# Performance work log

Measured on AMD Instinct MI355X. Metric: run time of the kernel, lower is better.

## Reference

```python
import jax, jax.numpy as jnp
import numpy as np

EPS = 1e-06


def setup_inputs() -> dict:
    key = jax.random.key(0)
    ks = jax.random.split(key, 6)
    B, L, N = 64, 4096, 128
    F = L // 2 + 1  # 2049 rfft bins
    E = 8
    x = jax.random.normal(ks[0], (B, L, N), dtype=jnp.float32)
    band_boundaries = jax.random.normal(ks[1], (E - 1,), dtype=jnp.float32)
    # gate: Linear(F,F) -> ReLU -> Linear(F,E); stored as [in,out] matrices
    gate_w1 = jax.random.normal(ks[2], (F, F), dtype=jnp.float32) * (1.0 / np.sqrt(F))
    gate_b1 = jnp.zeros((F,), dtype=jnp.float32)
    gate_w2 = jax.random.normal(ks[3], (F, E), dtype=jnp.float32) * (1.0 / np.sqrt(F))
    gate_b2 = jnp.zeros((E,), dtype=jnp.float32)
    return {"x": x, "band_boundaries": band_boundaries,
            "gate_w1": gate_w1, "gate_b1": gate_b1,
            "gate_w2": gate_w2, "gate_b2": gate_b2}


def reference(x, band_boundaries, gate_w1, gate_b1, gate_w2, gate_b2):
    # FrequencyMoE forward (residual_add=True). x: [B, L, N]
    B, L, N = x.shape
    F = L // 2 + 1
    xN = jnp.transpose(x, (0, 2, 1))  # [B, N, L]
    mean = jnp.mean(xN, axis=-1, keepdims=True)
    var = jnp.var(xN, axis=-1, keepdims=True) + EPS
    # NOTE: original code computes x_norm then overwrites with xN (normalization skipped),
    # but still rescales the reconstruction by sqrt(var) and adds mean back. Faithful copy.
    freq = jnp.fft.rfft(xN, n=L, axis=-1)  # [B, N, F] complex64

    # learnable band boundaries -> integer bin indices (non-differentiable, as in torch .long())
    bb = jnp.sort(jax.nn.sigmoid(band_boundaries))
    b01 = jnp.concatenate([jnp.zeros((1,), bb.dtype), bb, jnp.ones((1,), bb.dtype)])
    idx = jnp.clip((b01 * F).astype(jnp.int32), 0, F)
    idx = idx.at[-1].set(F)  # [E+1]

    bins = jnp.arange(F)
    # per-expert frequency masks [E, F]: bin in [idx[e], idx[e+1])
    masks = ((bins[None, :] >= idx[:-1, None]) & (bins[None, :] < idx[1:, None])).astype(xN.dtype)

    # gating on mean magnitude spectrum over variables
    mag = jnp.mean(jnp.abs(freq), axis=1)  # [B, F]
    h = jax.nn.relu(mag @ gate_w1 + gate_b1)
    weights = jax.nn.softmax(h @ gate_w2 + gate_b2, axis=-1)  # [B, E]

    # fused weighted-mask combination: sum_e w[b,e]*mask[e,f] applied to spectrum
    wmask = weights @ masks  # [B, F]
    freq_out = freq * wmask[:, None, :]
    x_rec = jnp.fft.irfft(freq_out, n=L, axis=-1)  # [B, N, L]
    x_rec = x_rec * jnp.sqrt(var) + mean
    outN = xN + x_rec  # residual_add=True
    return jnp.transpose(outN, (0, 2, 1))  # [B, L, N]
```

## Files before the change

### kernel.cpp

```cpp
#include <hip/hip_runtime.h>

#define B_ 64
#define L_ 4096
#define N_ 128
#define F_ 2049
#define M_ 2048

__device__ __forceinline__ int pidx(int a) { return a + (a >> 3); }

__device__ __forceinline__ float2 cadd(float2 a, float2 b) { return make_float2(a.x + b.x, a.y + b.y); }
__device__ __forceinline__ float2 csub(float2 a, float2 b) { return make_float2(a.x - b.x, a.y - b.y); }
__device__ __forceinline__ float2 cmul(float2 a, float2 b) {
  return make_float2(a.x * b.x - a.y * b.y, a.x * b.y + a.y * b.x);
}
template <int SGN>
__device__ __forceinline__ float2 mulsi(float2 a) {
  return (SGN > 0) ? make_float2(-a.y, a.x) : make_float2(a.y, -a.x);
}

template <int SGN>
__device__ __forceinline__ void dft8(float2* v) {
  const float C = 0.70710678118654752f;
  float2 t0 = cadd(v[0], v[4]), t1 = csub(v[0], v[4]);
  float2 t2 = cadd(v[2], v[6]), t3 = mulsi<SGN>(csub(v[2], v[6]));
  float2 t4 = cadd(v[1], v[5]), t5 = csub(v[1], v[5]);
  float2 t6 = cadd(v[3], v[7]), t7 = mulsi<SGN>(csub(v[3], v[7]));
  float2 u0 = cadd(t0, t2), u1 = csub(t0, t2);
  float2 u2 = cadd(t1, t3), u3 = csub(t1, t3);
  float2 u4 = cadd(t4, t6), u5 = csub(t4, t6);
  float2 u6 = cadd(t5, t7), u7 = csub(t5, t7);
  float2 w1 = make_float2(C, (SGN > 0) ? C : -C);
  float2 w3 = make_float2(-C, (SGN > 0) ? C : -C);
  float2 a5 = mulsi<SGN>(u5);
  float2 b6 = cmul(u6, w1);
  float2 b7 = cmul(u7, w3);
  v[0] = cadd(u0, u4); v[4] = csub(u0, u4);
  v[2] = cadd(u1, a5); v[6] = csub(u1, a5);
  v[1] = cadd(u2, b6); v[5] = csub(u2, b6);
  v[3] = cadd(u3, b7); v[7] = csub(u3, b7);
}

template <int SGN>
__device__ __forceinline__ void dft4(float2* v) {
  float2 e0 = cadd(v[0], v[2]), e1 = csub(v[0], v[2]);
  float2 o0 = cadd(v[1], v[3]), o1 = mulsi<SGN>(csub(v[1], v[3]));
  v[0] = cadd(e0, o0); v[2] = csub(e0, o0);
  v[1] = cadd(e1, o1); v[3] = csub(e1, o1);
}

template <int SGN>
__device__ __forceinline__ void tw8(float2* v, int pm) {
  float ang = (float)pm * 0.00306796157577128245f;
  float sv, cv;
  __sincosf(ang, &sv, &cv);
  float2 w = make_float2(cv, (SGN > 0) ? sv : -sv);
  float2 wk = w;
  v[1] = cmul(v[1], wk);
#pragma unroll
  for (int k = 2; k < 8; ++k) { wk = cmul(wk, w); v[k] = cmul(v[k], wk); }
}

template <int SGN>
__device__ __forceinline__ void fft2048(float2* __restrict__ buf, float2* v, int t) {
  dft8<SGN>(v);
  tw8<SGN>(v, t);
  __syncthreads();
#pragma unroll
  for (int k = 0; k < 8; ++k) buf[pidx(8 * t + k)] = v[k];
  __syncthreads();
#pragma unroll
  for (int r = 0; r < 8; ++r) v[r] = buf[pidx(t + 256 * r)];
  dft8<SGN>(v);
  tw8<SGN>(v, t & ~7);
  __syncthreads();
  {
    int q = t & 7, p = t >> 3;
#pragma unroll
    for (int k = 0; k < 8; ++k) buf[pidx(q + 8 * (8 * p + k))] = v[k];
  }
  __syncthreads();
#pragma unroll
  for (int r = 0; r < 8; ++r) v[r] = buf[pidx(t + 256 * r)];
  dft8<SGN>(v);
  tw8<SGN>(v, t & ~63);
  __syncthreads();
  {
    int q = t & 63, p = t >> 6;
#pragma unroll
    for (int k = 0; k < 8; ++k) buf[pidx(q + 64 * (8 * p + k))] = v[k];
  }
  __syncthreads();
  float2 w0[4], w1s[4];
#pragma unroll
  for (int r = 0; r < 4; ++r) {
    w0[r] = buf[pidx(t + 512 * r)];
    w1s[r] = buf[pidx(t + 256 + 512 * r)];
  }
  dft4<SGN>(w0);
  dft4<SGN>(w1s);
  __syncthreads();
#pragma unroll
  for (int k = 0; k < 4; ++k) {
    buf[pidx(t + 512 * k)] = w0[k];
    buf[pidx(t + 256 + 512 * k)] = w1s[k];
  }
  __syncthreads();
}

__global__ __launch_bounds__(256) void transpose4_k(const float* __restrict__ in,
                                                    float* __restrict__ out,
                                                    int R, int C) {
  __shared__ float tile[64][65];
  const float* ip = in + (size_t)blockIdx.z * R * C;
  float* op = out + (size_t)blockIdx.z * R * C;
  int c0 = blockIdx.x * 64;
  int r0 = blockIdx.y * 64;
  int t = threadIdx.x;
  {
    int fx = t & 15;
    int rq = t >> 4;
#pragma unroll
    for (int i = 0; i < 4; ++i) {
      int r = rq + 16 * i;
      float4 v = *(const float4*)&ip[(size_t)(r0 + r) * C + (c0 + 4 * fx)];
      tile[r][4 * fx + 0] = v.x;
      tile[r][4 * fx + 1] = v.y;
      tile[r][4 * fx + 2] = v.z;
      tile[r][4 * fx + 3] = v.w;
    }
  }
  __syncthreads();
  {
    int gm = t & 15;
    int cq = t >> 4;
#pragma unroll
    for (int i = 0; i < 4; ++i) {
      int c = cq + 16 * i;
      float4 v;
      v.x = tile[4 * gm + 0][c];
      v.y = tile[4 * gm + 1][c];
      v.z = tile[4 * gm + 2][c];
      v.w = tile[4 * gm + 3][c];
      *(float4*)&op[(size_t)(c0 + c) * R + (r0 + 4 * gm)] = v;
    }
  }
}

template <int S>
__global__ __launch_bounds__(256) void p1_fft_mag(const float* __restrict__ src,
                                                  float* __restrict__ magsum) {
  __shared__ float2 buf[2304];
  int t = threadIdx.x;
  int blk = blockIdx.x;
  int b = blk >> 7;
  int n = blk & 127;
  const float* base = (S == 1) ? (src + (size_t)blk * L_)
                               : (src + (size_t)b * L_ * N_ + n);
  float2 v[8];
  if (S == 1) {
    const float2* r2 = (const float2*)base;
#pragma unroll
    for (int r = 0; r < 8; ++r) v[r] = r2[t + 256 * r];
  } else {
#pragma unroll
    for (int r = 0; r < 8; ++r) {
      int k = t + 256 * r;
      v[r] = make_float2(base[(size_t)(2 * k) * S], base[(size_t)(2 * k + 1) * S]);
    }
  }
  fft2048<-1>(buf, v, t);

  float* msum = magsum + (size_t)b * F_;
#pragma unroll
  for (int i = 0; i < 8; ++i) {
    int f = t + 256 * i;
    float mg;
    if (f == 0) {
      float2 z = buf[pidx(0)];
      mg = fabsf(z.x + z.y);
      atomicAdd(&msum[2048], fabsf(z.x - z.y));
    } else {
      float2 zf = buf[pidx(f)], zm = buf[pidx(2048 - f)];
      float Are = 0.5f * (zf.x + zm.x), Aim = 0.5f * (zf.y - zm.y);
      float Bre = 0.5f * (zf.y + zm.y), Bim = -0.5f * (zf.x - zm.x);
      float ang = (float)f * 0.00153398078788564117f;
      float sv, cv;
      __sincosf(ang, &sv, &cv);
      float Xre = Are + cv * Bre + sv * Bim;
      float Xim = Aim + cv * Bim - sv * Bre;
      mg = sqrtf(Xre * Xre + Xim * Xim);
    }
    atomicAdd(&msum[f], mg);
  }
}

__global__ __launch_bounds__(256) void p1_fft_mag_z(const float* __restrict__ src,
                                                    float2* __restrict__ zout,
                                                    float* __restrict__ magsum) {
  __shared__ float2 buf[2304];
  int t = threadIdx.x;
  int blk = blockIdx.x;
  int b = blk >> 7;
  const float2* r2 = (const float2*)(src + (size_t)blk * L_);
  float2 v[8];
#pragma unroll
  for (int r = 0; r < 8; ++r) v[r] = r2[t + 256 * r];
  fft2048<-1>(buf, v, t);

  float* msum = magsum + (size_t)b * F_;
  float2* zrow = zout + (size_t)blk * (size_t)M_;
#pragma unroll
  for (int i = 0; i < 4; ++i) {
    int f = t + 256 * i;
    if (f == 0) {
      float2 z = buf[pidx(0)];
      float2 zc = buf[pidx(1024)];
      zrow[0] = z;
      zrow[1024] = zc;
      atomicAdd(&msum[0], fabsf(z.x + z.y));
      atomicAdd(&msum[2048], fabsf(z.x - z.y));
      atomicAdd(&msum[1024], sqrtf(zc.x * zc.x + zc.y * zc.y));
    } else {
      float2 zf = buf[pidx(f)], zm = buf[pidx(2048 - f)];
      zrow[f] = zf;
      zrow[2048 - f] = zm;
      float Are = 0.5f * (zf.x + zm.x), Aim = 0.5f * (zf.y - zm.y);
      float Bre = 0.5f * (zf.y + zm.y), Bim = -0.5f * (zf.x - zm.x);
      float ang = (float)f * 0.00153398078788564117f;
      float sv, cv;
      __sincosf(ang, &sv, &cv);
      float WBre = cv * Bre + sv * Bim;
      float WBim = cv * Bim - sv * Bre;
      float Xre = Are + WBre, Xim = Aim + WBim;
      float Xmre = Are - WBre, Xmim = Aim - WBim;
      atomicAdd(&msum[f], sqrtf(Xre * Xre + Xim * Xim));
      atomicAdd(&msum[2048 - f], sqrtf(Xmre * Xmre + Xmim * Xmim));
    }
  }
}

__global__ __launch_bounds__(256) void magt_k(const float* __restrict__ mag,
                                              float* __restrict__ magT) {
  int idx = blockIdx.x * 256 + threadIdx.x;
  if (idx >= 64 * F_) return;
  int f = idx >> 6, b = idx & 63;
  magT[idx] = mag[(size_t)b * F_ + f] * (1.0f / 128.0f);
}

#define G1K 33
__global__ __launch_bounds__(256) void g1_gemm(const float* __restrict__ magT,
                                               const float* __restrict__ W1,
                                               float* __restrict__ hsum) {
  int o = blockIdx.x * 256 + threadIdx.x;
  if (o >= F_) return;
  int i0 = blockIdx.y * G1K;
  int i1 = min(F_, i0 + G1K);
  float acc[64];
#pragma unroll
  for (int b = 0; b < 64; ++b) acc[b] = 0.f;
  for (int i = i0; i < i1; ++i) {
    float w = W1[(size_t)i * F_ + o];
    const float* mrow = magT + (size_t)i * 64;
#pragma unroll
    for (int b = 0; b < 64; ++b) acc[b] = fmaf(mrow[b], w, acc[b]);
  }
#pragma unroll
  for (int b = 0; b < 64; ++b) atomicAdd(&hsum[(size_t)b * F_ + o], acc[b]);
}

__global__ __launch_bounds__(256) void g2_gate(const float* __restrict__ hsum,
                                               const float* __restrict__ gb1,
                                               const float* __restrict__ W2,
                                               const float* __restrict__ gb2,
                                               const float* __restrict__ bbs,
                                               float* __restrict__ wmask) {
  __shared__ float red[256 * 8];
  __shared__ float wsm[8];
  __shared__ int idxs[9];
  int b = blockIdx.x;
  int t = threadIdx.x;
  float p[8];
#pragma unroll
  for (int e = 0; e < 8; ++e) p[e] = 0.f;
  for (int o = t; o < F_; o += 256) {
    float hv = hsum[(size_t)b * F_ + o] + gb1[o];
    hv = fmaxf(hv, 0.f);
    const float4* w2p = (const float4*)(W2 + (size_t)o * 8);
    float4 wa = w2p[0], wb = w2p[1];
    p[0] += hv * wa.x; p[1] += hv * wa.y; p[2] += hv * wa.z; p[3] += hv * wa.w;
    p[4] += hv * wb.x; p[5] += hv * wb.y; p[6] += hv * wb.z; p[7] += hv * wb.w;
  }
#pragma unroll
  for (int e = 0; e < 8; ++e) red[t * 8 + e] = p[e];
  __syncthreads();
  for (int s = 128; s >= 1; s >>= 1) {
    if (t < s) {
#pragma unroll
      for (int e = 0; e < 8; ++e) red[t * 8 + e] += red[(t + s) * 8 + e];
    }
    __syncthreads();
  }
  if (t == 0) {
    float lg[8];
    float mx = -1e30f;
#pragma unroll
    for (int e = 0; e < 8; ++e) { lg[e] = red[e] + gb2[e]; mx = fmaxf(mx, lg[e]); }
    float sm = 0.f;
#pragma unroll
    for (int e = 0; e < 8; ++e) { lg[e] = expf(lg[e] - mx); sm += lg[e]; }
    float inv = 1.f / sm;
#pragma unroll
    for (int e = 0; e < 8; ++e) wsm[e] = lg[e] * inv;
    float bv[7];
#pragma unroll
    for (int k = 0; k < 7; ++k) bv[k] = 1.f / (1.f + expf(-bbs[k]));
    for (int a = 1; a < 7; ++a) {
      float v = bv[a];
      int j = a - 1;
      while (j >= 0 && bv[j] > v) { bv[j + 1] = bv[j]; --j; }
      bv[j + 1] = v;
    }
    idxs[0] = 0;
    idxs[8] = F_;
    for (int k = 0; k < 7; ++k) {
      int v = (int)(bv[k] * (float)F_);
      v = min(max(v, 0), F_);
      idxs[k + 1] = v;
    }
  }
  __syncthreads();
  for (int f = t; f < F_; f += 256) {
    float wv = 0.f;
#pragma unroll
    for (int e = 0; e < 8; ++e)
      if (f >= idxs[e] && f < idxs[e + 1]) wv = wsm[e];
    wmask[(size_t)b * F_ + f] = wv;
  }
}

__global__ __launch_bounds__(256) void p3_filter_z(float2* __restrict__ zbuf,
                                                   const float* __restrict__ wmask) {
  __shared__ float2 buf[2304];
  __shared__ float rb[8];
  __shared__ float sstat[2];
  int t = threadIdx.x;
  int blk = blockIdx.x;
  int b = blk >> 7;
  float2* zrow = zbuf + (size_t)blk * (size_t)M_;
  float2 v[8];
  float lsq = 0.f;
#pragma unroll
  for (int r = 0; r < 8; ++r) {
    float2 z = zrow[t + 256 * r];
    v[r] = z;
    lsq += z.x * z.x + z.y * z.y;
  }
#pragma unroll
  for (int r = 0; r < 8; ++r) buf[pidx(t + 256 * r)] = v[r];
  for (int off = 32; off > 0; off >>= 1) lsq += __shfl_down(lsq, off);
  {
    int lane = t & 63, wid = t >> 6;
    if (lane == 0) rb[wid] = lsq;
  }
  __syncthreads();
  if (t == 0) {
    float s2 = rb[0] + rb[1] + rb[2] + rb[3];
    float2 z0 = buf[pidx(0)];
    float mean = (z0.x + z0.y) * (1.0f / 4096.0f);
    float sumsq = s2 * (1.0f / 2048.0f);
    float var = sumsq * (1.0f / 4096.0f) - mean * mean + 1e-6f;
    sstat[0] = mean;
    sstat[1] = sqrtf(var);
  }
  __syncthreads();

  float mean = sstat[0], sdv = sstat[1];
  const float* wm = wmask + (size_t)b * F_;

  float2 zf_[4], zm_[4];
#pragma unroll
  for (int i = 0; i < 4; ++i) {
    int f = t + 256 * i;
    int fm = (f == 0) ? 1024 : (2048 - f);
    zf_[i] = buf[pidx(f)];
    zm_[i] = buf[pidx(fm)];
  }
  __syncthreads();
#pragma unroll
  for (int i = 0; i < 4; ++i) {
    int f = t + 256 * i;
    if (f == 0) {
      float2 z0 = zf_[0];
      float2 zc = zm_[0];
      float X0 = (z0.x + z0.y) * (1.f + sdv * wm[0]);
      float XM = (z0.x - z0.y) * (1.f + sdv * wm[2048]);
      buf[pidx(0)] = make_float2(0.5f * (X0 + XM), 0.5f * (X0 - XM));
      float mc = 1.f + sdv * wm[1024];
      buf[pidx(1024)] = make_float2(zc.x * mc, zc.y * mc);
    } else {
      float2 zf = zf_[i], zm = zm_[i];
      float Are = 0.5f * (zf.x + zm.x), Aim = 0.5f * (zf.y - zm.y);
      float Bre = 0.5f * (zf.y + zm.y), Bim = -0.5f * (zf.x - zm.x);
      float ang = (float)f * 0.00153398078788564117f;
      float sv, cv;
      __sincosf(ang, &sv, &cv);
      float WBre = cv * Bre + sv * Bim;
      float WBim = cv * Bim - sv * Bre;
      float Xre = Are + WBre, Xim = Aim + WBim;
      float Xmre = Are - WBre, Xmim = -(Aim - WBim);
      float mf = 1.f + sdv * wm[f];
      float mg = 1.f + sdv * wm[2048 - f];
      Xre *= mf; Xim *= mf;
      Xmre *= mg; Xmim *= mg;
      float Apre = 0.5f * (Xre + Xmre), Apim = 0.5f * (Xim - Xmim);
      float Tre = 0.5f * (Xre - Xmre), Tim = 0.5f * (Xim + Xmim);
      float Bpre = cv * Tre - sv * Tim;
      float Bpim = cv * Tim + sv * Tre;
      buf[pidx(f)] = make_float2(Apre - Bpim, Apim + Bpre);
      float Agre = 0.5f * (Xmre + Xre), Agim = 0.5f * (Xmim - Xim);
      float Tgre = 0.5f * (Xmre - Xre), Tgim = 0.5f * (Xmim + Xim);
      float Bgre = -(cv * Tgre + sv * Tgim);
      float Bgim = -(cv * Tgim - sv * Tgre);
      buf[pidx(2048 - f)] = make_float2(Agre - Bgim, Agim + Bgre);
    }
  }
  __syncthreads();
#pragma unroll
  for (int r = 0; r < 8; ++r) v[r] = buf[pidx(t + 256 * r)];
  fft2048<1>(buf, v, t);

  const float inv = 1.0f / 2048.0f;
#pragma unroll
  for (int r = 0; r < 8; ++r) {
    int k = t + 256 * r;
    float2 z = buf[pidx(k)];
    zrow[k] = make_float2(z.x * inv + mean, z.y * inv + mean);
  }
}

template <int S>
__global__ __launch_bounds__(256) void p3_filter(const float* __restrict__ src,
                                                 const float* __restrict__ wmask,
                                                 float* __restrict__ dstp) {
  __shared__ float2 buf[2304];
  __shared__ float sstat[2];
  int t = threadIdx.x;
  int blk = blockIdx.x;
  int b = blk >> 7;
  int n = blk & 127;
  const float* base = (S == 1) ? (src + (size_t)blk * L_)
                               : (src + (size_t)b * L_ * N_ + n);
  float* obase = (S == 1) ? (dstp + (size_t)blk * L_)
                          : (dstp + (size_t)b * L_ * N_ + n);
  float2 v[8];
  float lsum = 0.f, lsq = 0.f;
  if (S == 1) {
    const float2* r2 = (const float2*)base;
#pragma unroll
    for (int r = 0; r < 8; ++r) {
      float2 z = r2[t + 256 * r];
      v[r] = z;
      lsum += z.x + z.y;
      lsq += z.x * z.x + z.y * z.y;
    }
  } else {
#pragma unroll
    for (int r = 0; r < 8; ++r) {
      int k = t + 256 * r;
      float2 z = make_float2(base[(size_t)(2 * k) * S], base[(size_t)(2 * k + 1) * S]);
      v[r] = z;
      lsum += z.x + z.y;
      lsq += z.x * z.x + z.y * z.y;
    }
  }
  for (int off = 32; off > 0; off >>= 1) {
    lsum += __shfl_down(lsum, off);
    lsq += __shfl_down(lsq, off);
  }
  {
    float* rb = (float*)buf;
    int lane = t & 63, wid = t >> 6;
    if (lane == 0) { rb[wid] = lsum; rb[8 + wid] = lsq; }
    __syncthreads();
    if (t == 0) {
      float s1 = rb[0] + rb[1] + rb[2] + rb[3];
      float s2 = rb[8] + rb[9] + rb[10] + rb[11];
      float mean = s1 * (1.0f / 4096.0f);
      float var = s2 * (1.0f / 4096.0f) - mean * mean + 1e-6f;
      sstat[0] = mean;
      sstat[1] = sqrtf(var);
    }
  }
  fft2048<-1>(buf, v, t);

  float mean = sstat[0], sdv = sstat[1];
  const float* wm = wmask + (size_t)b * F_;

  float2 zf_[4], zm_[4];
#pragma unroll
  for (int i = 0; i < 4; ++i) {
    int f = t + 256 * i;
    int fm = (f == 0) ? 1024 : (2048 - f);
    zf_[i] = buf[pidx(f)];
    zm_[i] = buf[pidx(fm)];
  }
  __syncthreads();
#pragma unroll
  for (int i = 0; i < 4; ++i) {
    int f = t + 256 * i;
    if (f == 0) {
      float2 z0 = zf_[0];
      float2 zc = zm_[0];
      float X0 = (z0.x + z0.y) * (1.f + sdv * wm[0]);
      float XM = (z0.x - z0.y) * (1.f + sdv * wm[2048]);
      buf[pidx(0)] = make_float2(0.5f * (X0 + XM), 0.5f * (X0 - XM));
      float mc = 1.f + sdv * wm[1024];
      buf[pidx(1024)] = make_float2(zc.x * mc, zc.y * mc);
    } else {
      float2 zf = zf_[i], zm = zm_[i];
      float Are = 0.5f * (zf.x + zm.x), Aim = 0.5f * (zf.y - zm.y);
      float Bre = 0.5f * (zf.y + zm.y), Bim = -0.5f * (zf.x - zm.x);
      float ang = (float)f * 0.00153398078788564117f;
      float sv, cv;
      __sincosf(ang, &sv, &cv);
      float WBre = cv * Bre + sv * Bim;
      float WBim = cv * Bim - sv * Bre;
      float Xre = Are + WBre, Xim = Aim + WBim;
      float Xmre = Are - WBre, Xmim = -(Aim - WBim);
      float mf = 1.f + sdv * wm[f];
      float mg = 1.f + sdv * wm[2048 - f];
      Xre *= mf; Xim *= mf;
      Xmre *= mg; Xmim *= mg;
      float Apre = 0.5f * (Xre + Xmre), Apim = 0.5f * (Xim - Xmim);
      float Tre = 0.5f * (Xre - Xmre), Tim = 0.5f * (Xim + Xmim);
      float Bpre = cv * Tre - sv * Tim;
      float Bpim = cv * Tim + sv * Tre;
      buf[pidx(f)] = make_float2(Apre - Bpim, Apim + Bpre);
      float Agre = 0.5f * (Xmre + Xre), Agim = 0.5f * (Xmim - Xim);
      float Tgre = 0.5f * (Xmre - Xre), Tgim = 0.5f * (Xmim + Xim);
      float Bgre = -(cv * Tgre + sv * Tgim);
      float Bgim = -(cv * Tgim - sv * Tgre);
      buf[pidx(2048 - f)] = make_float2(Agre - Bgim, Agim + Bgre);
    }
  }
  __syncthreads();
#pragma unroll
  for (int r = 0; r < 8; ++r) v[r] = buf[pidx(t + 256 * r)];
  fft2048<1>(buf, v, t);

  const float inv = 1.0f / 2048.0f;
  if (S == 1) {
    float2* o2 = (float2*)obase;
#pragma unroll
    for (int r = 0; r < 8; ++r) {
      int k = t + 256 * r;
      float2 z = buf[pidx(k)];
      o2[k] = make_float2(z.x * inv + mean, z.y * inv + mean);
    }
  } else {
#pragma unroll
    for (int r = 0; r < 8; ++r) {
      int k = t + 256 * r;
      float2 z = buf[pidx(k)];
      obase[(size_t)(2 * k) * S] = z.x * inv + mean;
      obase[(size_t)(2 * k + 1) * S] = z.y * inv + mean;
    }
  }
}

extern "C" void kernel_launch(void* const* d_in, const int* in_sizes, int n_in,
                              void* d_out, int out_size, void* d_ws,
                              size_t ws_size, hipStream_t stream) {
  const float* x = (const float*)d_in[0];
  const float* bbs = (const float*)d_in[1];
  const float* W1 = (const float*)d_in[2];
  const float* gb1 = (const float*)d_in[3];
  const float* W2 = (const float*)d_in[4];
  const float* gb2 = (const float*)d_in[5];
  float* out = (float*)d_out;

  const size_t bigElems = (size_t)B_ * N_ * L_;
  const size_t smallBytes = (size_t)3 * B_ * F_ * sizeof(float);
  const bool fast = ws_size >= bigElems * sizeof(float) + smallBytes;

  char* smallBase = (char*)d_ws + (fast ? bigElems * sizeof(float) : 0);
  float* magsum = (float*)smallBase;
  float* hsum = magsum + (size_t)B_ * F_;
  float* wmaskp = hsum + (size_t)B_ * F_;

  hipMemsetAsync(magsum, 0, (size_t)2 * B_ * F_ * sizeof(float), stream);

  const int g1x = (F_ + 255) / 256;
  const int g1y = (F_ + G1K - 1) / G1K;
  const int mtb = (64 * F_ + 255) / 256;
  if (fast) {
    float2* Z = (float2*)d_ws;
    transpose4_k<<<dim3(N_ / 64, L_ / 64, B_), 256, 0, stream>>>(x, out, L_, N_);
    p1_fft_mag_z<<<dim3(B_ * N_), 256, 0, stream>>>(out, Z, magsum);
    magt_k<<<dim3(mtb), 256, 0, stream>>>(magsum, wmaskp);
    g1_gemm<<<dim3(g1x, g1y), 256, 0, stream>>>(wmaskp, W1, hsum);
    g2_gate<<<dim3(B_), 256, 0, stream>>>(hsum, gb1, W2, gb2, bbs, wmaskp);
    p3_filter_z<<<dim3(B_ * N_), 256, 0, stream>>>(Z, wmaskp);
    transpose4_k<<<dim3(L_ / 64, N_ / 64, B_), 256, 0, stream>>>((float*)d_ws, out, N_, L_);
  } else {
    p1_fft_mag<N_><<<dim3(B_ * N_), 256, 0, stream>>>(x, magsum);
    magt_k<<<dim3(mtb), 256, 0, stream>>>(magsum, wmaskp);
    g1_gemm<<<dim3(g1x, g1y), 256, 0, stream>>>(wmaskp, W1, hsum);
    g2_gate<<<dim3(B_), 256, 0, stream>>>(hsum, gb1, W2, gb2, bbs, wmaskp);
    p3_filter<N_><<<dim3(B_ * N_), 256, 0, stream>>>(x, wmaskp, out);
  }
}
```

Measured before the change: 497.7 us.

## Process two FFT rows per block to share twiddles, syncs, and atomics

The forward and inverse FFT kernels now handle two rows per 256-thread block, interleaving two independent FFTs with shared twiddle computation and shared barriers. The magnitude atomics are combined across both rows, halving the atomic count, and the filter's separate register staging pass with its extra barrier is removed by operating in place on shared memory. This roughly doubles register and shared-memory use per block (launch bounds now request 4 blocks per CU) in exchange for more instruction-level parallelism and fewer barriers per row.

```diff
diff --git a/kernel.cpp b/kernel.cpp
--- a/kernel.cpp
+++ b/kernel.cpp
@@ -49,16 +49,20 @@
 }
 
 template <int SGN>
-__device__ __forceinline__ void tw8(float2* v, int pm) {
+__device__ __forceinline__ float2 twroot(int pm) {
   float ang = (float)pm * 0.00306796157577128245f;
   float sv, cv;
   __sincosf(ang, &sv, &cv);
-  float2 w = make_float2(cv, (SGN > 0) ? sv : -sv);
+  return make_float2(cv, (SGN > 0) ? sv : -sv);
+}
+__device__ __forceinline__ void tw8w(float2* v, float2 w) {
   float2 wk = w;
   v[1] = cmul(v[1], wk);
 #pragma unroll
   for (int k = 2; k < 8; ++k) { wk = cmul(wk, w); v[k] = cmul(v[k], wk); }
 }
+template <int SGN>
+__device__ __forceinline__ void tw8(float2* v, int pm) { tw8w(v, twroot<SGN>(pm)); }
 
 template <int SGN>
 __device__ __forceinline__ void fft2048(float2* __restrict__ buf, float2* v, int t) {
@@ -103,6 +107,63 @@
   for (int k = 0; k < 4; ++k) {
     buf[pidx(t + 512 * k)] = w0[k];
     buf[pidx(t + 256 + 512 * k)] = w1s[k];
+  }
+  __syncthreads();
+}
+
+template <int SGN>
+__device__ __forceinline__ void fft2048x2(float2* __restrict__ bufA, float2* __restrict__ bufB,
+                                          float2* va, float2* vb, int t) {
+  dft8<SGN>(va); dft8<SGN>(vb);
+  { float2 w = twroot<SGN>(t); tw8w(va, w); tw8w(vb, w); }
+  __syncthreads();
+#pragma unroll
+  for (int k = 0; k < 8; ++k) { bufA[pidx(8 * t + k)] = va[k]; bufB[pidx(8 * t + k)] = vb[k]; }
+  __syncthreads();
+#pragma unroll
+  for (int r = 0; r < 8; ++r) { va[r] = bufA[pidx(t + 256 * r)]; vb[r] = bufB[pidx(t + 256 * r)]; }
+  dft8<SGN>(va); dft8<SGN>(vb);
+  { float2 w = twroot<SGN>(t & ~7); tw8w(va, w); tw8w(vb, w); }
+  __syncthreads();
+  {
+    int q = t & 7, p = t >> 3;
+#pragma unroll
+    for (int k = 0; k < 8; ++k) {
+      int a = pidx(q + 8 * (8 * p + k));
+      bufA[a] = va[k]; bufB[a] = vb[k];
+    }
+  }
+  __syncthreads();
+#pragma unroll
+  for (int r = 0; r < 8; ++r) { va[r] = bufA[pidx(t + 256 * r)]; vb[r] = bufB[pidx(t + 256 * r)]; }
+  dft8<SGN>(va); dft8<SGN>(vb);
+  { float2 w = twroot<SGN>(t & ~63); tw8w(va, w); tw8w(vb, w); }
+  __syncthreads();
+  {
+    int q = t & 63, p = t >> 6;
+#pragma unroll
+    for (int k = 0; k < 8; ++k) {
+      int a = pidx(q + 64 * (8 * p + k));
+      bufA[a] = va[k]; bufB[a] = vb[k];
+    }
+  }
+  __syncthreads();
+  float2 wA0[4], wA1[4], wB0[4], wB1[4];
+#pragma unroll
+  for (int r = 0; r < 4; ++r) {
+    wA0[r] = bufA[pidx(t + 512 * r)];
+    wA1[r] = bufA[pidx(t + 256 + 512 * r)];
+    wB0[r] = bufB[pidx(t + 512 * r)];
+    wB1[r] = bufB[pidx(t + 256 + 512 * r)];
+  }
+  dft4<SGN>(wA0); dft4<SGN>(wA1); dft4<SGN>(wB0); dft4<SGN>(wB1);
+  __syncthreads();
+#pragma unroll
+  for (int k = 0; k < 4; ++k) {
+    bufA[pidx(t + 512 * k)] = wA0[k];
+    bufA[pidx(t + 256 + 512 * k)] = wA1[k];
+    bufB[pidx(t + 512 * k)] = wB0[k];
+    bufB[pidx(t + 256 + 512 * k)] = wB1[k];
   }
   __syncthreads();
 }
@@ -194,47 +255,60 @@
   }
 }
 
-__global__ __launch_bounds__(256) void p1_fft_mag_z(const float* __restrict__ src,
-                                                    float2* __restrict__ zout,
-                                                    float* __restrict__ magsum) {
-  __shared__ float2 buf[2304];
+__global__ __launch_bounds__(256, 4) void p1_fft_mag_z2(const float* __restrict__ src,
+                                                        float2* __restrict__ zout,
+                                                        float* __restrict__ magsum) {
+  __shared__ float2 bufA[2304];
+  __shared__ float2 bufB[2304];
   int t = threadIdx.x;
   int blk = blockIdx.x;
-  int b = blk >> 7;
-  const float2* r2 = (const float2*)(src + (size_t)blk * L_);
-  float2 v[8];
-#pragma unroll
-  for (int r = 0; r < 8; ++r) v[r] = r2[t + 256 * r];
-  fft2048<-1>(buf, v, t);
+  int b = blk >> 6;
+  const float2* rA = (const float2*)(src + (size_t)(2 * blk) * L_);
+  const float2* rB = rA + M_;
+  float2 va[8], vb[8];
+#pragma unroll
+  for (int r = 0; r < 8; ++r) { va[r] = rA[t + 256 * r]; vb[r] = rB[t + 256 * r]; }
+  fft2048x2<-1>(bufA, bufB, va, vb, t);
 
   float* msum = magsum + (size_t)b * F_;
-  float2* zrow = zout + (size_t)blk * (size_t)M_;
+  float2* zrA = zout + (size_t)(2 * blk) * (size_t)M_;
+  float2* zrB = zrA + M_;
 #pragma unroll
   for (int i = 0; i < 4; ++i) {
     int f = t + 256 * i;
     if (f == 0) {
-      float2 z = buf[pidx(0)];
-      float2 zc = buf[pidx(1024)];
-      zrow[0] = z;
-      zrow[1024] = zc;
-      atomicAdd(&msum[0], fabsf(z.x + z.y));
-      atomicAdd(&msum[2048], fabsf(z.x - z.y));
-      atomicAdd(&msum[1024], sqrtf(zc.x * zc.x + zc.y * zc.y));
+      float2 zA = bufA[pidx(0)], zcA = bufA[pidx(1024)];
+      float2 zB = bufB[pidx(0)], zcB = bufB[pidx(1024)];
+      zrA[0] = zA; zrA[1024] = zcA;
+      zrB[0] = zB; zrB[1024] = zcB;
+      atomicAdd(&msum[0], fabsf(zA.x + zA.y) + fabsf(zB.x + zB.y));
+      atomicAdd(&msum[2048], fabsf(zA.x - zA.y) + fabsf(zB.x - zB.y));
+      atomicAdd(&msum[1024], sqrtf(zcA.x * zcA.x + zcA.y * zcA.y) +
+                             sqrtf(zcB.x * zcB.x + zcB.y * zcB.y));
     } else {
-      float2 zf = buf[pidx(f)], zm = buf[pidx(2048 - f)];
-      zrow[f] = zf;
-      zrow[2048 - f] = zm;
-      float Are = 0.5f * (zf.x + zm.x), Aim = 0.5f * (zf.y - zm.y);
-      float Bre = 0.5f * (zf.y + zm.y), Bim = -0.5f * (zf.x - zm.x);
+      float2 zfA = bufA[pidx(f)], zmA = bufA[pidx(2048 - f)];
+      float2 zfB = bufB[pidx(f)], zmB = bufB[pidx(2048 - f)];
+      zrA[f] = zfA; zrA[2048 - f] = zmA;
+      zrB[f] = zfB; zrB[2048 - f] = zmB;
       float ang = (float)f * 0.00153398078788564117f;
       float sv, cv;
       __sincosf(ang, &sv, &cv);
+      float Are = 0.5f * (zfA.x + zmA.x), Aim = 0.5f * (zfA.y - zmA.y);
+      float Bre = 0.5f * (zfA.y + zmA.y), Bim = -0.5f * (zfA.x - zmA.x);
       float WBre = cv * Bre + sv * Bim;
       float WBim = cv * Bim - sv * Bre;
-      float Xre = Are + WBre, Xim = Aim + WBim;
-      float Xmre = Are - WBre, Xmim = Aim - WBim;
-      atomicAdd(&msum[f], sqrtf(Xre * Xre + Xim * Xim));
-      atomicAdd(&msum[2048 - f], sqrtf(Xmre * Xmre + Xmim * Xmim));
+      float XreA = Are + WBre, XimA = Aim + WBim;
+      float XmreA = Are - WBre, XmimA = Aim - WBim;
+      float Cre = 0.5f * (zfB.x + zmB.x), Cim = 0.5f * (zfB.y - zmB.y);
+      float Dre = 0.5f * (zfB.y + zmB.y), Dim = -0.5f * (zfB.x - zmB.x);
+      float WDre = cv * Dre + sv * Dim;
+      float WDim = cv * Dim - sv * Dre;
+      float XreB = Cre + WDre, XimB = Cim + WDim;
+      float XmreB = Cre - WDre, XmimB = Cim - WDim;
+      atomicAdd(&msum[f], sqrtf(XreA * XreA + XimA * XimA) +
+                          sqrtf(XreB * XreB + XimB * XimB));
+      atomicAdd(&msum[2048 - f], sqrtf(XmreA * XmreA + XmimA * XmimA) +
+                                 sqrtf(XmreB * XmreB + XmimB * XmimB));
     }
   }
 }
@@ -338,103 +412,134 @@
   }
 }
 
-__global__ __launch_bounds__(256) void p3_filter_z(float2* __restrict__ zbuf,
-                                                   const float* __restrict__ wmask) {
-  __shared__ float2 buf[2304];
-  __shared__ float rb[8];
-  __shared__ float sstat[2];
+__device__ __forceinline__ void filter_pair(float2& zf, float2& zm, int f,
+                                            float cv, float sv,
+                                            float mf, float mg) {
+  float Are = 0.5f * (zf.x + zm.x), Aim = 0.5f * (zf.y - zm.y);
+  float Bre = 0.5f * (zf.y + zm.y), Bim = -0.5f * (zf.x - zm.x);
+  float WBre = cv * Bre + sv * Bim;
+  float WBim = cv * Bim - sv * Bre;
+  float Xre = Are + WBre, Xim = Aim + WBim;
+  float Xmre = Are - WBre, Xmim = -(Aim - WBim);
+  Xre *= mf; Xim *= mf;
+  Xmre *= mg; Xmim *= mg;
+  float Apre = 0.5f * (Xre + Xmre), Apim = 0.5f * (Xim - Xmim);
+  float Tre = 0.5f * (Xre - Xmre), Tim = 0.5f * (Xim + Xmim);
+  float Bpre = cv * Tre - sv * Tim;
+  float Bpim = cv * Tim + sv * Tre;
+  zf = make_float2(Apre - Bpim, Apim + Bpre);
+  float Agre = 0.5f * (Xmre + Xre), Agim = 0.5f * (Xmim - Xim);
+  float Tgre = 0.5f * (Xmre - Xre), Tgim = 0.5f * (Xmim + Xim);
+  float Bgre = -(cv * Tgre + sv * Tgim);
+  float Bgim = -(cv * Tgim - sv * Tgre);
+  zm = make_float2(Agre - Bgim, Agim + Bgre);
+}
+
+__global__ __launch_bounds__(256, 4) void p3_filter_z2(float2* __restrict__ zbuf,
+                                                       const float* __restrict__ wmask) {
+  __shared__ float2 bufA[2304];
+  __shared__ float2 bufB[2304];
+  __shared__ float rb[16];
+  __shared__ float sstat[4];
   int t = threadIdx.x;
   int blk = blockIdx.x;
-  int b = blk >> 7;
-  float2* zrow = zbuf + (size_t)blk * (size_t)M_;
-  float2 v[8];
-  float lsq = 0.f;
+  int b = blk >> 6;
+  float2* zrA = zbuf + (size_t)(2 * blk) * (size_t)M_;
+  float2* zrB = zrA + M_;
+  float2 va[8], vb[8];
+  float lsqA = 0.f, lsqB = 0.f;
 #pragma unroll
   for (int r = 0; r < 8; ++r) {
-    float2 z = zrow[t + 256 * r];
-    v[r] = z;
-    lsq += z.x * z.x + z.y * z.y;
-  }
-#pragma unroll
-  for (int r = 0; r < 8; ++r) buf[pidx(t + 256 * r)] = v[r];
-  for (int off = 32; off > 0; off >>= 1) lsq += __shfl_down(lsq, off);
+    float2 zA = zrA[t + 256 * r];
+    float2 zB = zrB[t + 256 * r];
+    va[r] = zA; vb[r] = zB;
+    lsqA += zA.x * zA.x + zA.y * zA.y;
+    lsqB += zB.x * zB.x + zB.y * zB.y;
+  }
+#pragma unroll
+  for (int r = 0; r < 8; ++r) {
+    bufA[pidx(t + 256 * r)] = va[r];
+    bufB[pidx(t + 256 * r)] = vb[r];
+  }
+  for (int off = 32; off > 0; off >>= 1) {
+    lsqA += __shfl_down(lsqA, off);
+    lsqB += __shfl_down(lsqB, off);
+  }
   {
     int lane = t & 63, wid = t >> 6;
-    if (lane == 0) rb[wid] = lsq;
-  }
-  __syncthreads();
-  if (t == 0) {
-    float s2 = rb[0] + rb[1] + rb[2] + rb[3];
-    float2 z0 = buf[pidx(0)];
+    if (lane == 0) { rb[wid] = lsqA; rb[8 + wid] = lsqB; }
+  }
+  __syncthreads();
+  if (t < 2) {
+    const float* rr = rb + 8 * t;
+    float s2 = rr[0] + rr[1] + rr[2] + rr[3];
+    float2 z0 = (t == 0) ? bufA[pidx(0)] : bufB[pidx(0)];
     float mean = (z0.x + z0.y) * (1.0f / 4096.0f);
     float sumsq = s2 * (1.0f / 2048.0f);
     float var = sumsq * (1.0f / 4096.0f) - mean * mean + 1e-6f;
-    sstat[0] = mean;
-    sstat[1] = sqrtf(var);
-  }
-  __syncthreads();
-
-  float mean = sstat[0], sdv = sstat[1];
+    sstat[2 * t] = mean;
+    sstat[2 * t + 1] = sqrtf(var);
+  }
+  __syncthreads();
+
+  float meanA = sstat[0], sdvA = sstat[1];
+  float meanB = sstat[2], sdvB = sstat[3];
   const float* wm = wmask + (size_t)b * F_;
 
-  float2 zf_[4], zm_[4];
-#pragma unroll
-  for (int i = 0; i < 4; ++i) {
-    int f = t + 256 * i;
-    int fm = (f == 0) ? 1024 : (2048 - f);
-    zf_[i] = buf[pidx(f)];
-    zm_[i] = buf[pidx(fm)];
-  }
-  __syncthreads();
 #pragma unroll
   for (int i = 0; i < 4; ++i) {
     int f = t + 256 * i;
     if (f == 0) {
-      float2 z0 = zf_[0];
-      float2 zc = zm_[0];
-      float X0 = (z0.x + z0.y) * (1.f + sdv * wm[0]);
-      float XM = (z0.x - z0.y) * (1.f + sdv * wm[2048]);
-      buf[pidx(0)] = make_float2(0.5f * (X0 + XM), 0.5f * (X0 - XM));
-      float mc = 1.f + sdv * wm[1024];
-      buf[pidx(1024)] = make_float2(zc.x * mc, zc.y * mc);
+      float w0 = wm[0], wN = wm[2048], wC = wm[1024];
+      {
+        float2 z0 = bufA[pidx(0)], zc = bufA[pidx(1024)];
+        float X0 = (z0.x + z0.y) * (1.f + sdvA * w0);
+        float XM = (z0.x - z0.y) * (1.f + sdvA * wN);
+        bufA[pidx(0)] = make_float2(0.5f * (X0 + XM), 0.5f * (X0 - XM));
+        float mc = 1.f + sdvA * wC;
+        bufA[pidx(1024)] = make_float2(zc.x * mc, zc.y * mc);
+      }
+      {
+        float2 z0 = bufB[pidx(0)], zc = bufB[pidx(1024)];
+        float X0 = (z0.x + z0.y) * (1.f + sdvB * w0);
+        float XM = (z0.x - z0.y) * (1.f + sdvB * wN);
+        bufB[pidx(0)] = make_float2(0.5f * (X0 + XM), 0.5f * (X0 - XM));
+        float mc = 1.f + sdvB * wC;
+        bufB[pidx(1024)] = make_float2(zc.x * mc, zc.y * mc);
+      }
     } else {
-      float2 zf = zf_[i], zm = zm_[i];
-      float Are = 0.5f * (zf.x + zm.x), Aim = 0.5f * (zf.y - zm.y);
-      float Bre = 0.5f * (zf.y + zm.y), Bim = -0.5f * (zf.x - zm.x);
       float ang = (float)f * 0.00153398078788564117f;
       float sv, cv;
       __sincosf(ang, &sv, &cv);
-      float WBre = cv * Bre + sv * Bim;
-      float WBim = cv * Bim - sv * Bre;
-      float Xre = Are + WBre, Xim = Aim + WBim;
-      float Xmre = Are - WBre, Xmim = -(Aim - WBim);
-      float mf = 1.f + sdv * wm[f];
-      float mg = 1.f + sdv * wm[2048 - f];
-      Xre *= mf; Xim *= mf;
-      Xmre *= mg; Xmim *= mg;
-      float Apre = 0.5f * (Xre + Xmre), Apim = 0.5f * (Xim - Xmim);
-      float Tre = 0.5f * (Xre - Xmre), Tim = 0.5f * (Xim + Xmim);
-      float Bpre = cv * Tre - sv * Tim;
-      float Bpim = cv * Tim + sv * Tre;
-      buf[pidx(f)] = make_float2(Apre - Bpim, Apim + Bpre);
-      float Agre = 0.5f * (Xmre + Xre), Agim = 0.5f * (Xmim - Xim);
-      float Tgre = 0.5f * (Xmre - Xre), Tgim = 0.5f * (Xmim + Xim);
-      float Bgre = -(cv * Tgre + sv * Tgim);
-      float Bgim = -(cv * Tgim - sv * Tgre);
-      buf[pidx(2048 - f)] = make_float2(Agre - Bgim, Agim + Bgre);
-    }
-  }
-  __syncthreads();
-#pragma unroll
-  for (int r = 0; r < 8; ++r) v[r] = buf[pidx(t + 256 * r)];
-  fft2048<1>(buf, v, t);
+      float wf = wm[f], wg = wm[2048 - f];
+      {
+        float2 zf = bufA[pidx(f)], zm = bufA[pidx(2048 - f)];
+        filter_pair(zf, zm, f, cv, sv, 1.f + sdvA * wf, 1.f + sdvA * wg);
+        bufA[pidx(f)] = zf; bufA[pidx(2048 - f)] = zm;
+      }
+      {
+        float2 zf = bufB[pidx(f)], zm = bufB[pidx(2048 - f)];
+        filter_pair(zf, zm, f, cv, sv, 1.f + sdvB * wf, 1.f + sdvB * wg);
+        bufB[pidx(f)] = zf; bufB[pidx(2048 - f)] = zm;
+      }
+    }
+  }
+  __syncthreads();
+#pragma unroll
+  for (int r = 0; r < 8; ++r) {
+    va[r] = bufA[pidx(t + 256 * r)];
+    vb[r] = bufB[pidx(t + 256 * r)];
+  }
+  fft2048x2<1>(bufA, bufB, va, vb, t);
 
   const float inv = 1.0f / 2048.0f;
 #pragma unroll
   for (int r = 0; r < 8; ++r) {
     int k = t + 256 * r;
-    float2 z = buf[pidx(k)];
-    zrow[k] = make_float2(z.x * inv + mean, z.y * inv + mean);
+    float2 zA = bufA[pidx(k)];
+    float2 zB = bufB[pidx(k)];
+    zrA[k] = make_float2(zA.x * inv + meanA, zA.y * inv + meanA);
+    zrB[k] = make_float2(zB.x * inv + meanB, zB.y * inv + meanB);
   }
 }
 
@@ -496,51 +601,24 @@
   float mean = sstat[0], sdv = sstat[1];
   const float* wm = wmask + (size_t)b * F_;
 
-  float2 zf_[4], zm_[4];
-#pragma unroll
-  for (int i = 0; i < 4; ++i) {
-    int f = t + 256 * i;
-    int fm = (f == 0) ? 1024 : (2048 - f);
-    zf_[i] = buf[pidx(f)];
-    zm_[i] = buf[pidx(fm)];
-  }
-  __syncthreads();
 #pragma unroll
   for (int i = 0; i < 4; ++i) {
     int f = t + 256 * i;
     if (f == 0) {
-      float2 z0 = zf_[0];
-      float2 zc = zm_[0];
+      float2 z0 = buf[pidx(0)];
+      float2 zc = buf[pidx(1024)];
       float X0 = (z0.x + z0.y) * (1.f + sdv * wm[0]);
       float XM = (z0.x - z0.y) * (1.f + sdv * wm[2048]);
       buf[pidx(0)] = make_float2(0.5f * (X0 + XM), 0.5f * (X0 - XM));
       float mc = 1.f + sdv * wm[1024];
       buf[pidx(1024)] = make_float2(zc.x * mc, zc.y * mc);
     } else {
-      float2 zf = zf_[i], zm = zm_[i];
-      float Are = 0.5f * (zf.x + zm.x), Aim = 0.5f * (zf.y - zm.y);
-      float Bre = 0.5f * (zf.y + zm.y), Bim = -0.5f * (zf.x - zm.x);
       float ang = (float)f * 0.00153398078788564117f;
       float sv, cv;
       __sincosf(ang, &sv, &cv);
-      float WBre = cv * Bre + sv * Bim;
-      float WBim = cv * Bim - sv * Bre;
-      float Xre = Are + WBre, Xim = Aim + WBim;
-      float Xmre = Are - WBre, Xmim = -(Aim - WBim);
-      float mf = 1.f + sdv * wm[f];
-      float mg = 1.f + sdv * wm[2048 - f];
-      Xre *= mf; Xim *= mf;
-      Xmre *= mg; Xmim *= mg;
-      float Apre = 0.5f * (Xre + Xmre), Apim = 0.5f * (Xim - Xmim);
-      float Tre = 0.5f * (Xre - Xmre), Tim = 0.5f * (Xim + Xmim);
-      float Bpre = cv * Tre - sv * Tim;
-      float Bpim = cv * Tim + sv * Tre;
-      buf[pidx(f)] = make_float2(Apre - Bpim, Apim + Bpre);
-      float Agre = 0.5f * (Xmre + Xre), Agim = 0.5f * (Xmim - Xim);
-      float Tgre = 0.5f * (Xmre - Xre), Tgim = 0.5f * (Xmim + Xim);
-      float Bgre = -(cv * Tgre + sv * Tgim);
-      float Bgim = -(cv * Tgim - sv * Tgre);
-      buf[pidx(2048 - f)] = make_float2(Agre - Bgim, Agim + Bgre);
+      float2 zf = buf[pidx(f)], zm = buf[pidx(2048 - f)];
+      filter_pair(zf, zm, f, cv, sv, 1.f + sdv * wm[f], 1.f + sdv * wm[2048 - f]);
+      buf[pidx(f)] = zf; buf[pidx(2048 - f)] = zm;
     }
   }
   __syncthreads();
@@ -596,11 +674,11 @@
   if (fast) {
     float2* Z = (float2*)d_ws;
     transpose4_k<<<dim3(N_ / 64, L_ / 64, B_), 256, 0, stream>>>(x, out, L_, N_);
-    p1_fft_mag_z<<<dim3(B_ * N_), 256, 0, stream>>>(out, Z, magsum);
+    p1_fft_mag_z2<<<dim3(B_ * N_ / 2), 256, 0, stream>>>(out, Z, magsum);
     magt_k<<<dim3(mtb), 256, 0, stream>>>(magsum, wmaskp);
     g1_gemm<<<dim3(g1x, g1y), 256, 0, stream>>>(wmaskp, W1, hsum);
     g2_gate<<<dim3(B_), 256, 0, stream>>>(hsum, gb1, W2, gb2, bbs, wmaskp);
-    p3_filter_z<<<dim3(B_ * N_), 256, 0, stream>>>(Z, wmaskp);
+    p3_filter_z2<<<dim3(B_ * N_ / 2), 256, 0, stream>>>(Z, wmaskp);
     transpose4_k<<<dim3(L_ / 64, N_ / 64, B_), 256, 0, stream>>>((float*)d_ws, out, N_, L_);
   } else {
     p1_fft_mag<N_><<<dim3(B_ * N_), 256, 0, stream>>>(x, magsum);
```

Result: faster. 473.8 us (-4.8%).
